# Optimization experiments

Hardware: AMD Instinct MI355X
Metric: run time of the kernel (lower is better)

## Reference

```python
import jax, jax.numpy as jnp
import numpy as np

N_NODES = 50000
N_EDGES = 800000
F_IN = 128
HEADS = 4
OUT_C = 32
NEG_SLOPE = 0.2


def setup_inputs() -> dict:
    key = jax.random.key(0)
    ks = jax.random.split(key, 6)
    x = jax.random.normal(ks[0], (N_NODES, F_IN), dtype=jnp.float32)
    edge_index = jax.random.randint(ks[1], (2, N_EDGES), 0, N_NODES, dtype=jnp.int32)
    scale = 1.0 / np.sqrt(F_IN)
    W_l = jax.random.normal(ks[2], (F_IN, HEADS * OUT_C), dtype=jnp.float32) * scale
    W_r = jax.random.normal(ks[3], (F_IN, HEADS * OUT_C), dtype=jnp.float32) * scale
    b_l = jnp.zeros((HEADS * OUT_C,), dtype=jnp.float32)
    b_r = jnp.zeros((HEADS * OUT_C,), dtype=jnp.float32)
    att = jax.random.normal(ks[4], (1, HEADS, OUT_C), dtype=jnp.float32) * (1.0 / np.sqrt(OUT_C))
    bias = jnp.zeros((HEADS * OUT_C,), dtype=jnp.float32)
    return {"x": x, "edge_index": edge_index, "W_l": W_l, "b_l": b_l,
            "W_r": W_r, "b_r": b_r, "att": att, "bias": bias}


def reference(x, edge_index, W_l, b_l, W_r, b_r, att, bias):
    N = x.shape[0]
    H, C = HEADS, OUT_C
    src, dst = edge_index[0], edge_index[1]  # messages flow src(j) -> dst(i)

    x_l = (x @ W_l + b_l).reshape(N, H, C)  # Theta_t x (source/message transform)
    x_r = (x @ W_r + b_r).reshape(N, H, C)  # Theta_s x (target transform)

    # per-edge GATv2 score: a^T LeakyReLU(x_l[j] + x_r[i])
    e = x_l[src] + x_r[dst]                        # [E, H, C]
    e = jnp.where(e > 0, e, NEG_SLOPE * e)         # LeakyReLU
    alpha = jnp.sum(e * att, axis=-1)              # [E, H]

    # segment softmax over incoming edges of each dst node
    amax = jax.ops.segment_max(alpha, dst, num_segments=N)   # [N, H]
    amax = jnp.where(jnp.isfinite(amax), amax, 0.0)
    expa = jnp.exp(alpha - amax[dst])                        # [E, H]
    denom = jax.ops.segment_sum(expa, dst, num_segments=N)   # [N, H]
    alpha = expa / (denom[dst] + 1e-16)                      # [E, H]

    # scatter-aggregate messages: sum_j alpha_ij * x_l[j]
    msg = alpha[:, :, None] * x_l[src]                       # [E, H, C]
    out = jax.ops.segment_sum(msg, dst, num_segments=N)      # [N, H, C]
    out = out.reshape(N, H * C) + bias                       # concat heads + bias
    return out
```

## Files before the change

kernel.cpp:

```cpp
#include <hip/hip_runtime.h>
#include <math.h>

#define NNODES 50000
#define NEDGES 800000
#define FIN 128
#define HC 128
#define NHEADS 4
#define NEG 0.2f
#define CAP 64
#define GEMMB (((NNODES + 63) / 64) * 2)
#define HISTB ((NEDGES + 1023) / 1024)
#define ZB    ((NNODES + 255) / 256)
#define WTB   128

typedef _Float16 half8 __attribute__((ext_vector_type(8)));
typedef _Float16 half4v __attribute__((ext_vector_type(4)));
typedef float    f32x4 __attribute__((ext_vector_type(4)));

__global__ __launch_bounds__(256) void zero_wt_kernel(int* __restrict__ deg,
                                                      const float* __restrict__ Wl,
                                                      const float* __restrict__ Wr,
                                                      _Float16* __restrict__ Wt) {
    int t = threadIdx.x;
    if (blockIdx.x < ZB) {
        int i = blockIdx.x * 256 + t;
        if (i < NNODES) deg[i] = 0;
        return;
    }
    int flat = (blockIdx.x - ZB) * 256 + t;
    int k = flat >> 8, c = flat & 255;
    float v = (c < 128) ? Wl[(size_t)k * 128 + c] : Wr[(size_t)k * 128 + (c - 128)];
    Wt[(size_t)c * 128 + k] = (_Float16)v;
}

__global__ __launch_bounds__(256) void gemm_kernel(const float* __restrict__ x,
                                                   const _Float16* __restrict__ Wt,
                                                   const float* __restrict__ bl,
                                                   const float* __restrict__ br,
                                                   _Float16* __restrict__ xlh,
                                                   _Float16* __restrict__ xrh) {
    __shared__ _Float16 Asl[64 * 128];
    __shared__ _Float16 Bsl[128 * 128];
    int t = threadIdx.x;
    int nh = blockIdx.x & 1;
    int mb = blockIdx.x >> 1;

    {
        int row = t >> 2, q = t & 3;
        int node = mb * 64 + row;
        const float* xp = x + (size_t)(node < NNODES ? node : NNODES - 1) * FIN;
        float4 fa[8];
        #pragma unroll
        for (int uu = 0; uu < 4; ++uu) {
            fa[uu * 2]     = *(const float4*)(xp + (q * 4 + uu) * 8);
            fa[uu * 2 + 1] = *(const float4*)(xp + (q * 4 + uu) * 8 + 4);
        }
        #pragma unroll
        for (int uu = 0; uu < 4; ++uu) {
            int u = q * 4 + uu;
            float4 f0 = fa[uu * 2], f1 = fa[uu * 2 + 1];
            half8 h = { (_Float16)f0.x, (_Float16)f0.y, (_Float16)f0.z, (_Float16)f0.w,
                        (_Float16)f1.x, (_Float16)f1.y, (_Float16)f1.z, (_Float16)f1.w };
            *(half8*)&Asl[row * 128 + (u ^ (row & 7)) * 8] = h;
        }
        const _Float16* Wh = Wt + (size_t)nh * 128 * 128;
        half8 vb[8];
        #pragma unroll
        for (int i = 0; i < 8; ++i)
            vb[i] = *(const half8*)(Wh + (size_t)(t + i * 256) * 8);
        #pragma unroll
        for (int i = 0; i < 8; ++i) {
            int j = t + i * 256;
            int col = j >> 4, u = j & 15;
            *(half8*)&Bsl[col * 128 + (u ^ (col & 7)) * 8] = vb[i];
        }
    }
    __syncthreads();

    int wv = t >> 6, lane = t & 63;
    int ln15 = lane & 15, g = lane >> 4;
    const float* bb = nh ? br : bl;
    _Float16*    oo = nh ? xrh : xlh;

    float bias_v[8];
    #pragma unroll
    for (int nb = 0; nb < 8; ++nb)
        bias_v[nb] = bb[nb * 16 + ln15];

    half8 afrag[4];
    #pragma unroll
    for (int ks = 0; ks < 4; ++ks) {
        int rowa = wv * 16 + ln15;
        int ku = ks * 4 + g;
        afrag[ks] = *(half8*)&Asl[rowa * 128 + (ku ^ (rowa & 7)) * 8];
    }

    f32x4 acc[8];
    #pragma unroll
    for (int nb = 0; nb < 8; ++nb) acc[nb] = (f32x4){0.f, 0.f, 0.f, 0.f};

    #pragma unroll
    for (int ks = 0; ks < 4; ++ks) {
        int ku = ks * 4 + g;
        #pragma unroll
        for (int nb = 0; nb < 8; ++nb) {
            int col = nb * 16 + ln15;
            half8 bfrag = *(half8*)&Bsl[col * 128 + (ku ^ (col & 7)) * 8];
            acc[nb] = __builtin_amdgcn_mfma_f32_16x16x32_f16(afrag[ks], bfrag, acc[nb], 0, 0, 0);
        }
    }

    #pragma unroll
    for (int nb = 0; nb < 8; ++nb) {
        int cm = nb * 16 + ln15;
        #pragma unroll
        for (int i = 0; i < 4; ++i) {
            int node = mb * 64 + wv * 16 + g * 4 + i;
            if (node < NNODES)
                oo[(size_t)node * HC + cm] = (_Float16)(acc[nb][i] + bias_v[nb]);
        }
    }
}

__global__ __launch_bounds__(256) void hist_bucket_kernel(const int* __restrict__ src,
                                                          const int* __restrict__ dst,
                                                          int* __restrict__ deg,
                                                          unsigned short* __restrict__ bucket) {
    int base = (blockIdx.x * 256 + threadIdx.x) * 4;
    if (base + 3 < NEDGES) {
        int4 d = *(const int4*)(dst + base);
        int4 s = *(const int4*)(src + base);
        int p0 = atomicAdd(&deg[d.x], 1);
        int p1 = atomicAdd(&deg[d.y], 1);
        int p2 = atomicAdd(&deg[d.z], 1);
        int p3 = atomicAdd(&deg[d.w], 1);
        if (p0 < CAP) bucket[(size_t)d.x * CAP + p0] = (unsigned short)s.x;
        if (p1 < CAP) bucket[(size_t)d.y * CAP + p1] = (unsigned short)s.y;
        if (p2 < CAP) bucket[(size_t)d.z * CAP + p2] = (unsigned short)s.z;
        if (p3 < CAP) bucket[(size_t)d.w * CAP + p3] = (unsigned short)s.w;
    } else {
        for (int i = base; i < NEDGES; ++i) {
            int dd = dst[i];
            int p = atomicAdd(&deg[dd], 1);
            if (p < CAP) bucket[(size_t)dd * CAP + p] = (unsigned short)src[i];
        }
    }
}

__global__ __launch_bounds__(256) void fused_aggr_kernel(const int* __restrict__ deg,
                                                         const unsigned short* __restrict__ bucket,
                                                         const _Float16* __restrict__ xlh,
                                                         const _Float16* __restrict__ xrh,
                                                         const float* __restrict__ att,
                                                         const float* __restrict__ bias,
                                                         float* __restrict__ out) {
    int wid = threadIdx.x >> 6, lane = threadIdx.x & 63;
    int node = blockIdx.x * 4 + wid;
    if (node >= NNODES) return;
    int l32 = lane & 31, hl = lane >> 5;
    int c0 = l32 * 4;
    half4v xh = *(const half4v*)(xrh + (size_t)node * HC + c0);
    float4 xrv = make_float4((float)xh[0], (float)xh[1], (float)xh[2], (float)xh[3]);
    float4 atv = *(const float4*)(att + c0);
    float4 bv  = *(const float4*)(bias + c0);
    int dg = deg[node];
    dg = dg < CAP ? dg : CAP;
    int pbeg = node * CAP;
    int pend = pbeg + dg;
    float acc0 = 0.f, acc1 = 0.f, acc2 = 0.f, acc3 = 0.f, den = 0.f;

    #define EBODY(mh, valid)                                                   \
    {                                                                          \
        float m0 = (float)mh[0], m1 = (float)mh[1];                            \
        float m2 = (float)mh[2], m3 = (float)mh[3];                            \
        float a0 = m0 + xrv.x; a0 = a0 > 0.f ? a0 : NEG * a0;                  \
        float a1 = m1 + xrv.y; a1 = a1 > 0.f ? a1 : NEG * a1;                  \
        float a2 = m2 + xrv.z; a2 = a2 > 0.f ? a2 : NEG * a2;                  \
        float a3 = m3 + xrv.w; a3 = a3 > 0.f ? a3 : NEG * a3;                  \
        float pp = a0 * atv.x + a1 * atv.y + a2 * atv.z + a3 * atv.w;          \
        pp += __shfl_xor(pp, 1);                                               \
        pp += __shfl_xor(pp, 2);                                               \
        pp += __shfl_xor(pp, 4);                                               \
        float e = __expf(pp) * (valid);                                        \
        acc0 += e * m0; acc1 += e * m1; acc2 += e * m2; acc3 += e * m3;        \
        den += e;                                                              \
    }

    int p = pbeg;
    for (; p + 7 < pend; p += 8) {
        int s0 = bucket[p + hl],     s1 = bucket[p + 2 + hl];
        int s2 = bucket[p + 4 + hl], s3 = bucket[p + 6 + hl];
        half4v mh0 = *(const half4v*)(xlh + (size_t)s0 * HC + c0);
        half4v mh1 = *(const half4v*)(xlh + (size_t)s1 * HC + c0);
        half4v mh2 = *(const half4v*)(xlh + (size_t)s2 * HC + c0);
        half4v mh3 = *(const half4v*)(xlh + (size_t)s3 * HC + c0);
        EBODY(mh0, 1.f); EBODY(mh1, 1.f); EBODY(mh2, 1.f); EBODY(mh3, 1.f);
    }
    for (; p + 1 < pend; p += 2) {
        int s = bucket[p + hl];
        half4v mh = *(const half4v*)(xlh + (size_t)s * HC + c0);
        EBODY(mh, 1.f);
    }
    if (p < pend) {
        int s = bucket[p];
        half4v mh = *(const half4v*)(xlh + (size_t)s * HC + c0);
        EBODY(mh, hl ? 0.f : 1.f);
    }
    #undef EBODY

    acc0 += __shfl_xor(acc0, 32); acc1 += __shfl_xor(acc1, 32);
    acc2 += __shfl_xor(acc2, 32); acc3 += __shfl_xor(acc3, 32);
    den  += __shfl_xor(den, 32);

    if (hl == 0) {
        float inv = 1.0f / (den + 1e-16f);
        float4 o;
        o.x = acc0 * inv + bv.x;
        o.y = acc1 * inv + bv.y;
        o.z = acc2 * inv + bv.z;
        o.w = acc3 * inv + bv.w;
        *(float4*)(out + (size_t)node * HC + c0) = o;
    }
}

extern "C" void kernel_launch(void* const* d_in, const int* in_sizes, int n_in,
                              void* d_out, int out_size, void* d_ws, size_t ws_size,
                              hipStream_t stream) {
    const float* x    = (const float*)d_in[0];
    const int*   ei   = (const int*)  d_in[1];
    const float* Wl   = (const float*)d_in[2];
    const float* bl   = (const float*)d_in[3];
    const float* Wr   = (const float*)d_in[4];
    const float* br   = (const float*)d_in[5];
    const float* att  = (const float*)d_in[6];
    const float* bias = (const float*)d_in[7];
    float* out = (float*)d_out;

    _Float16* xlh = (_Float16*)d_ws;
    _Float16* xrh = xlh + (size_t)NNODES * HC;
    _Float16* Wt  = xrh + (size_t)NNODES * HC;
    int* deg = (int*)(Wt + 256 * 128);
    unsigned short* bucket = (unsigned short*)(deg + NNODES);

    const int* srcp = ei;
    const int* dstp = ei + NEDGES;

    zero_wt_kernel<<<ZB + WTB, 256, 0, stream>>>(deg, Wl, Wr, Wt);
    gemm_kernel<<<GEMMB, 256, 0, stream>>>(x, Wt, bl, br, xlh, xrh);
    hist_bucket_kernel<<<HISTB, 256, 0, stream>>>(srcp, dstp, deg, bucket);
    fused_aggr_kernel<<<(NNODES + 3) / 4, 256, 0, stream>>>(deg, bucket, xlh, xrh, att, bias, out);
}
```

Before: 127.1 us.

## Partition histogram/bucket scatter by destination range across blocks

The edge-bucketing kernel now launches 8 blocks per edge chunk. Each block handles only destinations within one eighth of the node range, so concurrently resident blocks' atomics and bucket writes fall in a narrower address window, which is meant to improve cache locality. The cost is that every edge is read 8 times and range checks are added. With blockIdx & 7 ordering, the adjacent blocks cover different ranges, so the locality benefit depends on how blocks are scheduled.

```diff
diff --git a/kernel.cpp b/kernel.cpp
--- a/kernel.cpp
+++ b/kernel.cpp
@@ -8,8 +8,10 @@
 #define NHEADS 4
 #define NEG 0.2f
 #define CAP 64
+#define RANGE ((NNODES + 7) / 8)
 #define GEMMB (((NNODES + 63) / 64) * 2)
-#define HISTB ((NEDGES + 1023) / 1024)
+#define HCHUNK ((NEDGES + 2047) / 2048)
+#define HISTB (HCHUNK * 8)
 #define ZB    ((NNODES + 255) / 256)
 #define WTB   128
 
@@ -126,25 +128,31 @@
                                                           const int* __restrict__ dst,
                                                           int* __restrict__ deg,
                                                           unsigned short* __restrict__ bucket) {
-    int base = (blockIdx.x * 256 + threadIdx.x) * 4;
-    if (base + 3 < NEDGES) {
-        int4 d = *(const int4*)(dst + base);
-        int4 s = *(const int4*)(src + base);
-        int p0 = atomicAdd(&deg[d.x], 1);
-        int p1 = atomicAdd(&deg[d.y], 1);
-        int p2 = atomicAdd(&deg[d.z], 1);
-        int p3 = atomicAdd(&deg[d.w], 1);
-        if (p0 < CAP) bucket[(size_t)d.x * CAP + p0] = (unsigned short)s.x;
-        if (p1 < CAP) bucket[(size_t)d.y * CAP + p1] = (unsigned short)s.y;
-        if (p2 < CAP) bucket[(size_t)d.z * CAP + p2] = (unsigned short)s.z;
-        if (p3 < CAP) bucket[(size_t)d.w * CAP + p3] = (unsigned short)s.w;
+    int r     = blockIdx.x & 7;
+    int chunk = blockIdx.x >> 3;
+    int rlo = r * RANGE, rhi = rlo + RANGE;
+    int base = (chunk * 256 + threadIdx.x) * 8;
+
+    #define COMMIT(d, s)                                                       \
+    if ((d) >= rlo && (d) < rhi) {                                             \
+        int p = atomicAdd(&deg[d], 1);                                         \
+        if (p < CAP) bucket[(size_t)(d) * CAP + p] = (unsigned short)(s);      \
+    }
+
+    if (base + 7 < NEDGES) {
+        int4 d0 = *(const int4*)(dst + base);
+        int4 d1 = *(const int4*)(dst + base + 4);
+        int4 s0 = *(const int4*)(src + base);
+        int4 s1 = *(const int4*)(src + base + 4);
+        COMMIT(d0.x, s0.x) COMMIT(d0.y, s0.y) COMMIT(d0.z, s0.z) COMMIT(d0.w, s0.w)
+        COMMIT(d1.x, s1.x) COMMIT(d1.y, s1.y) COMMIT(d1.z, s1.z) COMMIT(d1.w, s1.w)
     } else {
         for (int i = base; i < NEDGES; ++i) {
             int dd = dst[i];
-            int p = atomicAdd(&deg[dd], 1);
-            if (p < CAP) bucket[(size_t)dd * CAP + p] = (unsigned short)src[i];
-        }
-    }
+            COMMIT(dd, src[i])
+        }
+    }
+    #undef COMMIT
 }
 
 __global__ __launch_bounds__(256) void fused_aggr_kernel(const int* __restrict__ deg,
```

Result: faster. 111.1 us (-12.6%).
